# Optimization experiments

Measured on AMD Instinct MI355X. Metric: run time of the kernel, lower is better.

## Reference

```python
import jax, jax.numpy as jnp
import numpy as np


def setup_inputs() -> dict:
    key = jax.random.key(0)
    x = jax.random.normal(key, (64, 256, 56, 56), dtype=jnp.float32)
    return {"x": x}


def reference(x):
    # x: [B, C, H, W]. Computes BN stats (mean/var over [0,2,3]) and
    # GroupNorm-style stats for group sizes 2, 4, 8, 16 channels
    # (i.e. views [B, C//g, g*H*W]). All vars are biased (unbiased=False).
    B, C, H, W = x.shape
    hw = H * W
    # Single pass over x: per-(batch, channel) sum and sum-of-squares.
    s = x.sum(axis=(2, 3))            # [B, C]
    ss = (x * x).sum(axis=(2, 3))     # [B, C]

    # BatchNorm stats over [0, 2, 3]
    n_bn = B * hw
    mean_bn = s.sum(axis=0) / n_bn                      # [C]
    var_bn = ss.sum(axis=0) / n_bn - mean_bn * mean_bn  # [C]

    def group_stats(s_g, ss_g, g):
        # combine g adjacent channels per group, hierarchically
        s2 = s_g.reshape(B, -1, 2).sum(-1)
        ss2 = ss_g.reshape(B, -1, 2).sum(-1)
        n = g * hw
        m = s2 / n
        v = ss2 / n - m * m
        return s2, ss2, m, v

    s2, ss2, m2, v2 = group_stats(s, ss, 2)      # [B, C//2]
    s4, ss4, m4, v4 = group_stats(s2, ss2, 4)    # [B, C//4]
    s8, ss8, m8, v8 = group_stats(s4, ss4, 8)    # [B, C//8]
    _, _, m16, v16 = group_stats(s8, ss8, 16)    # [B, C//16]

    # Original forward returns x; stats are side-effect buffers, so we
    # expose them in the output tuple for correctness checking.
    return (x, mean_bn, var_bn, m2, v2, m4, v4, m8, v8, m16, v16)
```

## Files before the change

kernel.cpp:

```cpp
#include <hip/hip_runtime.h>

#define BB 64
#define CC 256
#define HW 3136
#define VEC (HW / 4)
#define NROW (BB * CC)

typedef float f32x4 __attribute__((ext_vector_type(4)));

__global__ __launch_bounds__(256) void reduce_copy_kernel(
    const float* __restrict__ x, float* __restrict__ out,
    float* __restrict__ s_ws, float* __restrict__ ss_ws) {
  const int row  = blockIdx.x * 4 + (threadIdx.x >> 6);
  const int lane = threadIdx.x & 63;
  const size_t base = (size_t)row * HW;
  const f32x4* __restrict__ xv = (const f32x4*)(x + base);
  f32x4* __restrict__ ov = (f32x4*)(out + base);

  f32x4 v0, v1, v2, v3, v4, v5, v6, v7, v8, v9, v10, v11, vt;
  v0  = __builtin_nontemporal_load(&xv[lane +  0 * 64]);
  v1  = __builtin_nontemporal_load(&xv[lane +  1 * 64]);
  v2  = __builtin_nontemporal_load(&xv[lane +  2 * 64]);
  v3  = __builtin_nontemporal_load(&xv[lane +  3 * 64]);
  v4  = __builtin_nontemporal_load(&xv[lane +  4 * 64]);
  v5  = __builtin_nontemporal_load(&xv[lane +  5 * 64]);
  v6  = __builtin_nontemporal_load(&xv[lane +  6 * 64]);
  v7  = __builtin_nontemporal_load(&xv[lane +  7 * 64]);
  v8  = __builtin_nontemporal_load(&xv[lane +  8 * 64]);
  v9  = __builtin_nontemporal_load(&xv[lane +  9 * 64]);
  v10 = __builtin_nontemporal_load(&xv[lane + 10 * 64]);
  v11 = __builtin_nontemporal_load(&xv[lane + 11 * 64]);
  const bool tail = lane < 16;
  if (tail) vt = __builtin_nontemporal_load(&xv[768 + lane]);

  float s = 0.f, ss = 0.f;
#define STEP(V, IDX)                                            \
  __builtin_nontemporal_store(V, &ov[IDX]);                     \
  s += V.x + V.y + V.z + V.w;                                   \
  ss += V.x * V.x + V.y * V.y + V.z * V.z + V.w * V.w;
  STEP(v0,  lane +  0 * 64)
  STEP(v1,  lane +  1 * 64)
  STEP(v2,  lane +  2 * 64)
  STEP(v3,  lane +  3 * 64)
  STEP(v4,  lane +  4 * 64)
  STEP(v5,  lane +  5 * 64)
  STEP(v6,  lane +  6 * 64)
  STEP(v7,  lane +  7 * 64)
  STEP(v8,  lane +  8 * 64)
  STEP(v9,  lane +  9 * 64)
  STEP(v10, lane + 10 * 64)
  STEP(v11, lane + 11 * 64)
  if (tail) {
    STEP(vt, 768 + lane)
  }
#undef STEP

  for (int off = 32; off; off >>= 1) {
    s += __shfl_down(s, off, 64);
    ss += __shfl_down(ss, off, 64);
  }
  if (lane == 0) {
    s_ws[row]  = s;
    ss_ws[row] = ss;
  }
}

__global__ __launch_bounds__(256) void stats_kernel(
    const float* __restrict__ s_ws, const float* __restrict__ ss_ws,
    float* __restrict__ out) {
  const size_t OX = (size_t)NROW * HW;
  float* mean_bn = out + OX;
  float* var_bn  = mean_bn + CC;
  float* m2  = var_bn + CC;
  float* v2  = m2 + BB * (CC / 2);
  float* m4  = v2 + BB * (CC / 2);
  float* v4  = m4 + BB * (CC / 4);
  float* m8  = v4 + BB * (CC / 4);
  float* v8  = m8 + BB * (CC / 8);
  float* m16 = v8 + BB * (CC / 8);
  float* v16 = m16 + BB * (CC / 16);

  const int b = blockIdx.x;
  const int t = threadIdx.x;

  if (b == BB) {
    float S = 0.f, SS = 0.f;
    for (int bb = 0; bb < BB; ++bb) {
      S += s_ws[bb * CC + t];
      SS += ss_ws[bb * CC + t];
    }
    const float inv_n = 1.f / ((float)BB * (float)HW);
    const float m = S * inv_n;
    mean_bn[t] = m;
    var_bn[t]  = SS * inv_n - m * m;
    return;
  }

  __shared__ float ls2[128], lss2[128];
  __shared__ float ls4[64],  lss4[64];
  __shared__ float ls8[32],  lss8[32];

  if (t < 128) {
    float s2  = s_ws[b * CC + 2 * t] + s_ws[b * CC + 2 * t + 1];
    float ss2 = ss_ws[b * CC + 2 * t] + ss_ws[b * CC + 2 * t + 1];
    ls2[t] = s2; lss2[t] = ss2;
    const float inv_n = 1.f / (2.f * HW);
    const float m = s2 * inv_n;
    m2[b * 128 + t] = m;
    v2[b * 128 + t] = ss2 * inv_n - m * m;
  }
  __syncthreads();
  if (t < 64) {
    float s4  = ls2[2 * t] + ls2[2 * t + 1];
    float ss4 = lss2[2 * t] + lss2[2 * t + 1];
    ls4[t] = s4; lss4[t] = ss4;
    const float inv_n = 1.f / (4.f * HW);
    const float m = s4 * inv_n;
    m4[b * 64 + t] = m;
    v4[b * 64 + t] = ss4 * inv_n - m * m;
  }
  __syncthreads();
  if (t < 32) {
    float s8  = ls4[2 * t] + ls4[2 * t + 1];
    float ss8 = lss4[2 * t] + lss4[2 * t + 1];
    ls8[t] = s8; lss8[t] = ss8;
    const float inv_n = 1.f / (8.f * HW);
    const float m = s8 * inv_n;
    m8[b * 32 + t] = m;
    v8[b * 32 + t] = ss8 * inv_n - m * m;
  }
  __syncthreads();
  if (t < 16) {
    float s16  = ls8[2 * t] + ls8[2 * t + 1];
    float ss16 = lss8[2 * t] + lss8[2 * t + 1];
    const float inv_n = 1.f / (16.f * HW);
    const float m = s16 * inv_n;
    m16[b * 16 + t] = m;
    v16[b * 16 + t] = ss16 * inv_n - m * m;
  }
}

extern "C" void kernel_launch(void* const* d_in, const int* in_sizes, int n_in,
                              void* d_out, int out_size, void* d_ws, size_t ws_size,
                              hipStream_t stream) {
  const float* x = (const float*)d_in[0];
  float* out = (float*)d_out;
  float* s_ws = (float*)d_ws;
  float* ss_ws = s_ws + NROW;

  reduce_copy_kernel<<<NROW / 4, 256, 0, stream>>>(x, out, s_ws, ss_ws);
  stats_kernel<<<BB + 1, 256, 0, stream>>>(s_ws, ss_ws, out);
}
```

Measured before the change: 74.89 us.

## Fuse reduce-copy and group stats into one kernel with last-block BN reduction

```diff
diff --git a/kernel.cpp b/kernel.cpp
--- a/kernel.cpp
+++ b/kernel.cpp
@@ -3,140 +3,152 @@
 #define BB 64
 #define CC 256
 #define HW 3136
-#define VEC (HW / 4)
+#define VEC4 (HW / 4)
 #define NROW (BB * CC)
+#define NBLK (BB * 16)
 
 typedef float f32x4 __attribute__((ext_vector_type(4)));
 
-__global__ __launch_bounds__(256) void reduce_copy_kernel(
+__global__ __launch_bounds__(256) void fused_kernel(
     const float* __restrict__ x, float* __restrict__ out,
-    float* __restrict__ s_ws, float* __restrict__ ss_ws) {
-  const int row  = blockIdx.x * 4 + (threadIdx.x >> 6);
+    float* __restrict__ s_ws, float* __restrict__ ss_ws,
+    unsigned int* __restrict__ cnt) {
+  const int b    = blockIdx.x >> 4;
+  const int cg   = blockIdx.x & 15;
+  const int wv   = threadIdx.x >> 6;
   const int lane = threadIdx.x & 63;
-  const size_t base = (size_t)row * HW;
-  const f32x4* __restrict__ xv = (const f32x4*)(x + base);
-  f32x4* __restrict__ ov = (f32x4*)(out + base);
+  const int t    = threadIdx.x;
 
-  f32x4 v0, v1, v2, v3, v4, v5, v6, v7, v8, v9, v10, v11, vt;
-  v0  = __builtin_nontemporal_load(&xv[lane +  0 * 64]);
-  v1  = __builtin_nontemporal_load(&xv[lane +  1 * 64]);
-  v2  = __builtin_nontemporal_load(&xv[lane +  2 * 64]);
-  v3  = __builtin_nontemporal_load(&xv[lane +  3 * 64]);
-  v4  = __builtin_nontemporal_load(&xv[lane +  4 * 64]);
-  v5  = __builtin_nontemporal_load(&xv[lane +  5 * 64]);
-  v6  = __builtin_nontemporal_load(&xv[lane +  6 * 64]);
-  v7  = __builtin_nontemporal_load(&xv[lane +  7 * 64]);
-  v8  = __builtin_nontemporal_load(&xv[lane +  8 * 64]);
-  v9  = __builtin_nontemporal_load(&xv[lane +  9 * 64]);
-  v10 = __builtin_nontemporal_load(&xv[lane + 10 * 64]);
-  v11 = __builtin_nontemporal_load(&xv[lane + 11 * 64]);
-  const bool tail = lane < 16;
-  if (tail) vt = __builtin_nontemporal_load(&xv[768 + lane]);
+  __shared__ float s_l[16], ss_l[16];
+  __shared__ float s2l[8], ss2l[8], s4l[4], ss4l[4], s8l[2], ss8l[2];
+  __shared__ bool last;
 
-  float s = 0.f, ss = 0.f;
+#pragma unroll
+  for (int r = 0; r < 4; ++r) {
+    const int ch_in_blk = wv * 4 + r;
+    const size_t base = ((size_t)(b * CC + cg * 16 + ch_in_blk)) * HW;
+    const f32x4* __restrict__ xv = (const f32x4*)(x + base);
+    f32x4* __restrict__ ov = (f32x4*)(out + base);
+
+    f32x4 v0, v1, v2, v3, v4, v5, v6, v7, v8, v9, v10, v11, vt;
+    v0  = __builtin_nontemporal_load(&xv[lane +  0 * 64]);
+    v1  = __builtin_nontemporal_load(&xv[lane +  1 * 64]);
+    v2  = __builtin_nontemporal_load(&xv[lane +  2 * 64]);
+    v3  = __builtin_nontemporal_load(&xv[lane +  3 * 64]);
+    v4  = __builtin_nontemporal_load(&xv[lane +  4 * 64]);
+    v5  = __builtin_nontemporal_load(&xv[lane +  5 * 64]);
+    v6  = __builtin_nontemporal_load(&xv[lane +  6 * 64]);
+    v7  = __builtin_nontemporal_load(&xv[lane +  7 * 64]);
+    v8  = __builtin_nontemporal_load(&xv[lane +  8 * 64]);
+    v9  = __builtin_nontemporal_load(&xv[lane +  9 * 64]);
+    v10 = __builtin_nontemporal_load(&xv[lane + 10 * 64]);
+    v11 = __builtin_nontemporal_load(&xv[lane + 11 * 64]);
+    const bool tail = lane < 16;
+    if (tail) vt = __builtin_nontemporal_load(&xv[768 + lane]);
+
+    float s = 0.f, ss = 0.f;
 #define STEP(V, IDX)                                            \
-  __builtin_nontemporal_store(V, &ov[IDX]);                     \
-  s += V.x + V.y + V.z + V.w;                                   \
-  ss += V.x * V.x + V.y * V.y + V.z * V.z + V.w * V.w;
-  STEP(v0,  lane +  0 * 64)
-  STEP(v1,  lane +  1 * 64)
-  STEP(v2,  lane +  2 * 64)
-  STEP(v3,  lane +  3 * 64)
-  STEP(v4,  lane +  4 * 64)
-  STEP(v5,  lane +  5 * 64)
-  STEP(v6,  lane +  6 * 64)
-  STEP(v7,  lane +  7 * 64)
-  STEP(v8,  lane +  8 * 64)
-  STEP(v9,  lane +  9 * 64)
-  STEP(v10, lane + 10 * 64)
-  STEP(v11, lane + 11 * 64)
-  if (tail) {
-    STEP(vt, 768 + lane)
-  }
+    __builtin_nontemporal_store(V, &ov[IDX]);                   \
+    s += V.x + V.y + V.z + V.w;                                 \
+    ss += V.x * V.x + V.y * V.y + V.z * V.z + V.w * V.w;
+    STEP(v0,  lane +  0 * 64)
+    STEP(v1,  lane +  1 * 64)
+    STEP(v2,  lane +  2 * 64)
+    STEP(v3,  lane +  3 * 64)
+    STEP(v4,  lane +  4 * 64)
+    STEP(v5,  lane +  5 * 64)
+    STEP(v6,  lane +  6 * 64)
+    STEP(v7,  lane +  7 * 64)
+    STEP(v8,  lane +  8 * 64)
+    STEP(v9,  lane +  9 * 64)
+    STEP(v10, lane + 10 * 64)
+    STEP(v11, lane + 11 * 64)
+    if (tail) {
+      STEP(vt, 768 + lane)
+    }
 #undef STEP
 
-  for (int off = 32; off; off >>= 1) {
-    s += __shfl_down(s, off, 64);
-    ss += __shfl_down(ss, off, 64);
+    for (int off = 32; off; off >>= 1) {
+      s += __shfl_down(s, off, 64);
+      ss += __shfl_down(ss, off, 64);
+    }
+    if (lane == 0) { s_l[ch_in_blk] = s; ss_l[ch_in_blk] = ss; }
   }
-  if (lane == 0) {
-    s_ws[row]  = s;
-    ss_ws[row] = ss;
-  }
-}
+  __syncthreads();
 
-__global__ __launch_bounds__(256) void stats_kernel(
-    const float* __restrict__ s_ws, const float* __restrict__ ss_ws,
-    float* __restrict__ out) {
   const size_t OX = (size_t)NROW * HW;
   float* mean_bn = out + OX;
   float* var_bn  = mean_bn + CC;
   float* m2  = var_bn + CC;
-  float* v2  = m2 + BB * (CC / 2);
-  float* m4  = v2 + BB * (CC / 2);
-  float* v4  = m4 + BB * (CC / 4);
-  float* m8  = v4 + BB * (CC / 4);
-  float* v8  = m8 + BB * (CC / 8);
-  float* m16 = v8 + BB * (CC / 8);
-  float* v16 = m16 + BB * (CC / 16);
+  float* v2o = m2 + BB * 128;
+  float* m4  = v2o + BB * 128;
+  float* v4o = m4 + BB * 64;
+  float* m8  = v4o + BB * 64;
+  float* v8o = m8 + BB * 32;
+  float* m16 = v8o + BB * 32;
+  float* v16 = m16 + BB * 16;
 
-  const int b = blockIdx.x;
-  const int t = threadIdx.x;
+  if (t < 16) {
+    s_ws[b * CC + cg * 16 + t]  = s_l[t];
+    ss_ws[b * CC + cg * 16 + t] = ss_l[t];
+  }
 
-  if (b == BB) {
+  if (t < 8) {
+    float s2 = s_l[2 * t] + s_l[2 * t + 1];
+    float q2 = ss_l[2 * t] + ss_l[2 * t + 1];
+    s2l[t] = s2; ss2l[t] = q2;
+    const float inv = 1.f / (2.f * HW);
+    const float m = s2 * inv;
+    m2[b * 128 + cg * 8 + t]  = m;
+    v2o[b * 128 + cg * 8 + t] = q2 * inv - m * m;
+  }
+  __syncthreads();
+  if (t < 4) {
+    float s4 = s2l[2 * t] + s2l[2 * t + 1];
+    float q4 = ss2l[2 * t] + ss2l[2 * t + 1];
+    s4l[t] = s4; ss4l[t] = q4;
+    const float inv = 1.f / (4.f * HW);
+    const float m = s4 * inv;
+    m4[b * 64 + cg * 4 + t]  = m;
+    v4o[b * 64 + cg * 4 + t] = q4 * inv - m * m;
+  }
+  __syncthreads();
+  if (t < 2) {
+    float s8 = s4l[2 * t] + s4l[2 * t + 1];
+    float q8 = ss4l[2 * t] + ss4l[2 * t + 1];
+    s8l[t] = s8; ss8l[t] = q8;
+    const float inv = 1.f / (8.f * HW);
+    const float m = s8 * inv;
+    m8[b * 32 + cg * 2 + t]  = m;
+    v8o[b * 32 + cg * 2 + t] = q8 * inv - m * m;
+  }
+  __syncthreads();
+  if (t == 0) {
+    float s16 = s8l[0] + s8l[1];
+    float q16 = ss8l[0] + ss8l[1];
+    const float inv = 1.f / (16.f * HW);
+    const float m = s16 * inv;
+    m16[b * 16 + cg] = m;
+    v16[b * 16 + cg] = q16 * inv - m * m;
+  }
+  __syncthreads();
+
+  if (t == 0) {
+    __threadfence();
+    last = (atomicAdd(cnt, 1u) == (unsigned)(NBLK - 1));
+  }
+  __syncthreads();
+  if (last) {
+    __threadfence();
     float S = 0.f, SS = 0.f;
     for (int bb = 0; bb < BB; ++bb) {
-      S += s_ws[bb * CC + t];
+      S  += s_ws[bb * CC + t];
       SS += ss_ws[bb * CC + t];
     }
-    const float inv_n = 1.f / ((float)BB * (float)HW);
-    const float m = S * inv_n;
+    const float inv = 1.f / ((float)BB * (float)HW);
+    const float m = S * inv;
     mean_bn[t] = m;
-    var_bn[t]  = SS * inv_n - m * m;
-    return;
-  }
-
-  __shared__ float ls2[128], lss2[128];
-  __shared__ float ls4[64],  lss4[64];
-  __shared__ float ls8[32],  lss8[32];
-
-  if (t < 128) {
-    float s2  = s_ws[b * CC + 2 * t] + s_ws[b * CC + 2 * t + 1];
-    float ss2 = ss_ws[b * CC + 2 * t] + ss_ws[b * CC + 2 * t + 1];
-    ls2[t] = s2; lss2[t] = ss2;
-    const float inv_n = 1.f / (2.f * HW);
-    const float m = s2 * inv_n;
-    m2[b * 128 + t] = m;
-    v2[b * 128 + t] = ss2 * inv_n - m * m;
-  }
-  __syncthreads();
-  if (t < 64) {
-    float s4  = ls2[2 * t] + ls2[2 * t + 1];
-    float ss4 = lss2[2 * t] + lss2[2 * t + 1];
-    ls4[t] = s4; lss4[t] = ss4;
-    const float inv_n = 1.f / (4.f * HW);
-    const float m = s4 * inv_n;
-    m4[b * 64 + t] = m;
-    v4[b * 64 + t] = ss4 * inv_n - m * m;
-  }
-  __syncthreads();
-  if (t < 32) {
-    float s8  = ls4[2 * t] + ls4[2 * t + 1];
-    float ss8 = lss4[2 * t] + lss4[2 * t + 1];
-    ls8[t] = s8; lss8[t] = ss8;
-    const float inv_n = 1.f / (8.f * HW);
-    const float m = s8 * inv_n;
-    m8[b * 32 + t] = m;
-    v8[b * 32 + t] = ss8 * inv_n - m * m;
-  }
-  __syncthreads();
-  if (t < 16) {
-    float s16  = ls8[2 * t] + ls8[2 * t + 1];
-    float ss16 = lss8[2 * t] + lss8[2 * t + 1];
-    const float inv_n = 1.f / (16.f * HW);
-    const float m = s16 * inv_n;
-    m16[b * 16 + t] = m;
-    v16[b * 16 + t] = ss16 * inv_n - m * m;
+    var_bn[t]  = SS * inv - m * m;
   }
 }
 
@@ -147,7 +159,8 @@
   float* out = (float*)d_out;
   float* s_ws = (float*)d_ws;
   float* ss_ws = s_ws + NROW;
+  unsigned int* cnt = (unsigned int*)(ss_ws + NROW);
 
-  reduce_copy_kernel<<<NROW / 4, 256, 0, stream>>>(x, out, s_ws, ss_ws);
-  stats_kernel<<<BB + 1, 256, 0, stream>>>(s_ws, ss_ws, out);
+  hipMemsetAsync(cnt, 0, sizeof(unsigned int), stream);
+  fused_kernel<<<NBLK, 256, 0, stream>>>(x, out, s_ws, ss_ws, cnt);
 }
```

Result: slower. 143.1 us (+91.0%).
